# Performance work log

Hardware: AMD Instinct MI355X
Metric: run time of the kernel (lower is better)

The kernel has to match this reference:

```python
import jax, jax.numpy as jnp
import numpy as np

PAD = 1      # init_kwargs: padding
STRIDE = 1   # init_kwargs: stride


def setup_inputs() -> dict:
    key = jax.random.key(0)
    k1, k2 = jax.random.split(key)
    # x: [C=4, H=4096, W=4096] input feature map (no batch dim in original module)
    x = jax.random.normal(k1, (4, 4096, 4096), dtype=jnp.float32)
    # kernel: [cout=4, cin=4, h=3, w=3] learned conv weight (nn.Parameter)
    kernel = jax.random.normal(k2, (4, 4, 3, 3), dtype=jnp.float32)
    return {"x": x, "kernel": kernel}


def reference(x, kernel):
    # Faithful math: zero-pad by PAD on all four spatial sides, then a direct
    # cross-correlation (torch conv semantics) with stride STRIDE.
    # Original loops over output pixels; here it's a single fused conv primitive.
    out = jax.lax.conv_general_dilated(
        x[None],                      # [1, C, H, W]
        kernel,                       # [cout, cin, h, w]
        window_strides=(STRIDE, STRIDE),
        padding=[(PAD, PAD), (PAD, PAD)],
        dimension_numbers=("NCHW", "OIHW", "NCHW"),
    )
    return out[0]                     # [cout, hout, wout]
```

## Files before the change

kernel.cpp:

```cpp
#include <hip/hip_runtime.h>


#define IW 4096
#define IH 4096
constexpr long long HWsz = (long long)IH * IW;

typedef float v4f __attribute__((ext_vector_type(4)));

#define LROW 1028

__device__ __forceinline__ void gload_lds16(const float* g, float* l) {
    __builtin_amdgcn_global_load_lds(
        (const __attribute__((address_space(1))) char*)g,
        (__attribute__((address_space(3))) char*)l, 16, 0, 0);
}
__device__ __forceinline__ void gload_lds4(const float* g, float* l) {
    __builtin_amdgcn_global_load_lds(
        (const __attribute__((address_space(1))) char*)g,
        (__attribute__((address_space(3))) char*)l, 4, 0, 0);
}

__device__ __forceinline__ void stage(const float* __restrict__ xin, int ci,
                                      float (*rbuf)[LROW], float* hbuf,
                                      int y0, int X0, int w, int l) {
    const float* plane = xin + (long long)ci * HWsz;
    const int xg = X0 + 256 * w + 4 * l;
    #pragma unroll
    for (int r = 0; r < 6; ++r) {
        int yy = y0 - 1 + r;
        int yc = yy < 0 ? 0 : (yy >= IH ? IH - 1 : yy);
        gload_lds16(plane + (long long)yc * IW + xg, &rbuf[r][256 * w]);
    }
    if (l < 3) {
        const int s   = 3 * w + l;
        const int r   = s >> 1;
        const int sid = s & 1;
        int yy = y0 - 1 + r;
        int yc = yy < 0 ? 0 : (yy >= IH ? IH - 1 : yy);
        int x  = sid ? (X0 + 1024) : (X0 - 1);
        int xc = x < 0 ? 0 : (x >= IW ? IW - 1 : x);
        gload_lds4(plane + (long long)yc * IW + xc, &hbuf[3 * w]);
    }
}

__device__ __forceinline__ void compute_ci(float acc[4][4][4],
                                           const float (*rbuf)[LROW],
                                           const float* hbuf,
                                           const float* __restrict__ wt, int ci,
                                           int y0, int t, bool xlo, bool xhi) {
    #pragma unroll
    for (int dy = 0; dy < 6; ++dy) {
        const int yy = y0 - 1 + dy;
        if (yy >= 0 && yy < IH) {
            const v4f a = *reinterpret_cast<const v4f*>(&rbuf[dy][4 * t]);
            float L = (t == 0)   ? hbuf[2 * dy]     : rbuf[dy][4 * t - 1];
            float R = (t == 255) ? hbuf[2 * dy + 1] : rbuf[dy][4 * t + 4];
            if (t == 0 && xlo)   L = 0.f;
            if (t == 255 && xhi) R = 0.f;
            float vv[6] = {L, a.x, a.y, a.z, a.w, R};
            #pragma unroll
            for (int rk = 0; rk < 3; ++rk) {
                const int o = dy - rk;
                if (o >= 0 && o < 4) {
                    #pragma unroll
                    for (int co = 0; co < 4; ++co) {
                        #pragma unroll
                        for (int kx = 0; kx < 3; ++kx) {
                            const float w = wt[((co * 4 + ci) * 3 + rk) * 3 + kx];
                            #pragma unroll
                            for (int p = 0; p < 4; ++p)
                                acc[o][co][p] = fmaf(w, vv[p + kx], acc[o][co][p]);
                        }
                    }
                }
            }
        }
    }
}

__global__ __launch_bounds__(256) void conv3x3_kernel(
    const float* __restrict__ xin,
    const float* __restrict__ wt,
    float* __restrict__ out)
{
    __shared__ __align__(16) float rows[2][6][LROW];
    __shared__ float halo[2][12];

    const int bid = blockIdx.x;
    const int swz = (bid & 7) * 512 + (bid >> 3);
    const int rowblk = swz >> 2;
    const int xq     = swz & 3;
    const int y0     = rowblk << 2;
    const int X0     = xq << 10;
    const int t      = (int)threadIdx.x;
    const int w      = t >> 6, l = t & 63;
    const bool xlo   = (X0 == 0);
    const bool xhi   = (X0 + 1024 == IW);

    float acc[4][4][4];
    #pragma unroll
    for (int o = 0; o < 4; ++o)
        #pragma unroll
        for (int co = 0; co < 4; ++co)
            #pragma unroll
            for (int p = 0; p < 4; ++p) acc[o][co][p] = 0.f;

    stage(xin, 0, rows[0], halo[0], y0, X0, w, l);

    #pragma unroll 1
    for (int ci = 0; ci < 4; ++ci) {
        const int cur = ci & 1;
        if (ci < 3) {
            stage(xin, ci + 1, rows[cur ^ 1], halo[cur ^ 1], y0, X0, w, l);
            asm volatile("s_waitcnt vmcnt(7)\n\ts_barrier" ::: "memory");
        } else {
            asm volatile("s_waitcnt vmcnt(0)\n\ts_barrier" ::: "memory");
        }
        compute_ci(acc, rows[cur], halo[cur], wt, ci, y0, t, xlo, xhi);
        if (ci < 3)
            asm volatile("s_barrier" ::: "memory");
    }

    const int x0g = X0 + 4 * t;
    #pragma unroll
    for (int o = 0; o < 4; ++o) {
        const long long obase = (long long)(y0 + o) * IW + x0g;
        #pragma unroll
        for (int co = 0; co < 4; ++co) {
            v4f ov;
            ov.x = acc[o][co][0]; ov.y = acc[o][co][1];
            ov.z = acc[o][co][2]; ov.w = acc[o][co][3];
            __builtin_nontemporal_store(ov,
                reinterpret_cast<v4f*>(out + co * HWsz + obase));
        }
    }
}

extern "C" void kernel_launch(void* const* d_in, const int* in_sizes, int n_in,
                              void* d_out, int out_size, void* d_ws, size_t ws_size,
                              hipStream_t stream) {
    const float* xin = (const float*)d_in[0];
    const float* wt  = (const float*)d_in[1];
    float* out       = (float*)d_out;

    dim3 grid(4096), block(256);
    hipLaunchKernelGGL(conv3x3_kernel, grid, block, 0, stream, xin, wt, out);
}
```

Baseline: 97.87 us.

## Give each wavefront private LDS staging buffers and drop block barriers

The shared 1024-wide LDS row buffer is split into four 256-wide per-wavefront buffers, and each wave now loads its own halo columns. Because no wave reads another wave's data, the s_barrier calls are replaced by per-wave waitcnts, so waves no longer stall on each other between input channels. In exchange each wave loads extra halo elements, and correctness now depends on waitcnt ordering within a wave instead of block barriers.

```diff
diff --git a/kernel.cpp b/kernel.cpp
--- a/kernel.cpp
+++ b/kernel.cpp
@@ -6,8 +6,6 @@
 constexpr long long HWsz = (long long)IH * IW;
 
 typedef float v4f __attribute__((ext_vector_type(4)));
-
-#define LROW 1028
 
 __device__ __forceinline__ void gload_lds16(const float* g, float* l) {
     __builtin_amdgcn_global_load_lds(
@@ -21,42 +19,40 @@
 }
 
 __device__ __forceinline__ void stage(const float* __restrict__ xin, int ci,
-                                      float (*rbuf)[LROW], float* hbuf,
-                                      int y0, int X0, int w, int l) {
+                                      float (*rbuf)[256], float* hbuf,
+                                      int y0, int xw, int l) {
     const float* plane = xin + (long long)ci * HWsz;
-    const int xg = X0 + 256 * w + 4 * l;
     #pragma unroll
     for (int r = 0; r < 6; ++r) {
         int yy = y0 - 1 + r;
         int yc = yy < 0 ? 0 : (yy >= IH ? IH - 1 : yy);
-        gload_lds16(plane + (long long)yc * IW + xg, &rbuf[r][256 * w]);
+        gload_lds16(plane + (long long)yc * IW + (xw + 4 * l), &rbuf[r][0]);
     }
-    if (l < 3) {
-        const int s   = 3 * w + l;
-        const int r   = s >> 1;
-        const int sid = s & 1;
+    if (l < 12) {
+        const int r   = l >> 1;
+        const int sid = l & 1;
         int yy = y0 - 1 + r;
         int yc = yy < 0 ? 0 : (yy >= IH ? IH - 1 : yy);
-        int x  = sid ? (X0 + 1024) : (X0 - 1);
+        int x  = sid ? (xw + 256) : (xw - 1);
         int xc = x < 0 ? 0 : (x >= IW ? IW - 1 : x);
-        gload_lds4(plane + (long long)yc * IW + xc, &hbuf[3 * w]);
+        gload_lds4(plane + (long long)yc * IW + xc, &hbuf[0]);
     }
 }
 
 __device__ __forceinline__ void compute_ci(float acc[4][4][4],
-                                           const float (*rbuf)[LROW],
+                                           const float (*rbuf)[256],
                                            const float* hbuf,
                                            const float* __restrict__ wt, int ci,
-                                           int y0, int t, bool xlo, bool xhi) {
+                                           int y0, int l, bool xlo, bool xhi) {
     #pragma unroll
     for (int dy = 0; dy < 6; ++dy) {
         const int yy = y0 - 1 + dy;
         if (yy >= 0 && yy < IH) {
-            const v4f a = *reinterpret_cast<const v4f*>(&rbuf[dy][4 * t]);
-            float L = (t == 0)   ? hbuf[2 * dy]     : rbuf[dy][4 * t - 1];
-            float R = (t == 255) ? hbuf[2 * dy + 1] : rbuf[dy][4 * t + 4];
-            if (t == 0 && xlo)   L = 0.f;
-            if (t == 255 && xhi) R = 0.f;
+            const v4f a = *reinterpret_cast<const v4f*>(&rbuf[dy][4 * l]);
+            const float L = (l == 0)  ? (xlo ? 0.f : hbuf[2 * dy])
+                                      : rbuf[dy][4 * l - 1];
+            const float R = (l == 63) ? (xhi ? 0.f : hbuf[2 * dy + 1])
+                                      : rbuf[dy][4 * l + 4];
             float vv[6] = {L, a.x, a.y, a.z, a.w, R};
             #pragma unroll
             for (int rk = 0; rk < 3; ++rk) {
@@ -83,8 +79,8 @@
     const float* __restrict__ wt,
     float* __restrict__ out)
 {
-    __shared__ __align__(16) float rows[2][6][LROW];
-    __shared__ float halo[2][12];
+    __shared__ __align__(16) float rows[4][2][6][256];
+    __shared__ float halo[4][2][12];
 
     const int bid = blockIdx.x;
     const int swz = (bid & 7) * 512 + (bid >> 3);
@@ -94,8 +90,9 @@
     const int X0     = xq << 10;
     const int t      = (int)threadIdx.x;
     const int w      = t >> 6, l = t & 63;
-    const bool xlo   = (X0 == 0);
-    const bool xhi   = (X0 + 1024 == IW);
+    const int xw     = X0 + 256 * w;
+    const bool xlo   = (xw == 0);
+    const bool xhi   = (xw + 256 == IW);
 
     float acc[4][4][4];
     #pragma unroll
@@ -105,20 +102,19 @@
             #pragma unroll
             for (int p = 0; p < 4; ++p) acc[o][co][p] = 0.f;
 
-    stage(xin, 0, rows[0], halo[0], y0, X0, w, l);
+    stage(xin, 0, rows[w][0], halo[w][0], y0, xw, l);
 
     #pragma unroll 1
     for (int ci = 0; ci < 4; ++ci) {
         const int cur = ci & 1;
         if (ci < 3) {
-            stage(xin, ci + 1, rows[cur ^ 1], halo[cur ^ 1], y0, X0, w, l);
-            asm volatile("s_waitcnt vmcnt(7)\n\ts_barrier" ::: "memory");
+            asm volatile("s_waitcnt lgkmcnt(0)" ::: "memory");
+            stage(xin, ci + 1, rows[w][cur ^ 1], halo[w][cur ^ 1], y0, xw, l);
+            asm volatile("s_waitcnt vmcnt(7)" ::: "memory");
         } else {
-            asm volatile("s_waitcnt vmcnt(0)\n\ts_barrier" ::: "memory");
+            asm volatile("s_waitcnt vmcnt(0)" ::: "memory");
         }
-        compute_ci(acc, rows[cur], halo[cur], wt, ci, y0, t, xlo, xhi);
-        if (ci < 3)
-            asm volatile("s_barrier" ::: "memory");
+        compute_ci(acc, rows[w][cur], halo[w][cur], wt, ci, y0, l, xlo, xhi);
     }
 
     const int x0g = X0 + 4 * t;
```

New measurement: 104.9 us. +7.2%, slower.

## Retile conv to 8x512 blocks and fetch halo columns directly from global

Applied to the files above, without the earlier changes.

Each block now covers 8 output rows by 512 columns instead of 4 rows by 1024 columns. Each half of the block computes 4 rows from a shared 10-row LDS staging buffer. Before, every 4 output rows needed 6 input rows; now every 8 output rows need 10, which lowers redundant input reads. The separate LDS halo staging is dropped; each wave loads the left and right halo pixels straight from global memory inside the compute loop, using wave-uniform addresses. This simplifies staging, but it adds global loads on the compute path that may stall it.

```diff
diff --git a/kernel.cpp b/kernel.cpp
--- a/kernel.cpp
+++ b/kernel.cpp
@@ -7,56 +7,47 @@
 
 typedef float v4f __attribute__((ext_vector_type(4)));
 
-#define LROW 1028
-
 __device__ __forceinline__ void gload_lds16(const float* g, float* l) {
     __builtin_amdgcn_global_load_lds(
         (const __attribute__((address_space(1))) char*)g,
         (__attribute__((address_space(3))) char*)l, 16, 0, 0);
 }
-__device__ __forceinline__ void gload_lds4(const float* g, float* l) {
-    __builtin_amdgcn_global_load_lds(
-        (const __attribute__((address_space(1))) char*)g,
-        (__attribute__((address_space(3))) char*)l, 4, 0, 0);
-}
 
 __device__ __forceinline__ void stage(const float* __restrict__ xin, int ci,
-                                      float (*rbuf)[LROW], float* hbuf,
-                                      int y0, int X0, int w, int l) {
+                                      float (*rbuf)[512], int y0, int X0,
+                                      int w, int l) {
     const float* plane = xin + (long long)ci * HWsz;
-    const int xg = X0 + 256 * w + 4 * l;
     #pragma unroll
-    for (int r = 0; r < 6; ++r) {
+    for (int k = 0; k < 5; ++k) {
+        const int c = 5 * w + k;
+        const int r = c >> 1;
+        const int h = c & 1;
         int yy = y0 - 1 + r;
         int yc = yy < 0 ? 0 : (yy >= IH ? IH - 1 : yy);
-        gload_lds16(plane + (long long)yc * IW + xg, &rbuf[r][256 * w]);
-    }
-    if (l < 3) {
-        const int s   = 3 * w + l;
-        const int r   = s >> 1;
-        const int sid = s & 1;
-        int yy = y0 - 1 + r;
-        int yc = yy < 0 ? 0 : (yy >= IH ? IH - 1 : yy);
-        int x  = sid ? (X0 + 1024) : (X0 - 1);
-        int xc = x < 0 ? 0 : (x >= IW ? IW - 1 : x);
-        gload_lds4(plane + (long long)yc * IW + xc, &hbuf[3 * w]);
+        gload_lds16(plane + (long long)yc * IW + (X0 + 256 * h + 4 * l),
+                    &rbuf[r][256 * h]);
     }
 }
 
 __device__ __forceinline__ void compute_ci(float acc[4][4][4],
-                                           const float (*rbuf)[LROW],
-                                           const float* hbuf,
-                                           const float* __restrict__ wt, int ci,
-                                           int y0, int t, bool xlo, bool xhi) {
+                                           const float (*rbuf)[512],
+                                           const float* __restrict__ xin,
+                                           const float* __restrict__ wt,
+                                           int ci, int y0, int X0,
+                                           int p_u, int tx) {
+    const float* plane = xin + (long long)ci * HWsz;
     #pragma unroll
     for (int dy = 0; dy < 6; ++dy) {
-        const int yy = y0 - 1 + dy;
+        const int r  = 4 * p_u + dy;
+        const int yy = y0 - 1 + r;
         if (yy >= 0 && yy < IH) {
-            const v4f a = *reinterpret_cast<const v4f*>(&rbuf[dy][4 * t]);
-            float L = (t == 0)   ? hbuf[2 * dy]     : rbuf[dy][4 * t - 1];
-            float R = (t == 255) ? hbuf[2 * dy + 1] : rbuf[dy][4 * t + 4];
-            if (t == 0 && xlo)   L = 0.f;
-            if (t == 255 && xhi) R = 0.f;
+            const float hL = (X0 > 0)
+                ? plane[(long long)yy * IW + X0 - 1]   : 0.f;
+            const float hR = (X0 + 512 < IW)
+                ? plane[(long long)yy * IW + X0 + 512] : 0.f;
+            const v4f a = *reinterpret_cast<const v4f*>(&rbuf[r][4 * tx]);
+            const float L = (tx == 0)   ? hL : rbuf[r][4 * tx - 1];
+            const float R = (tx == 127) ? hR : rbuf[r][4 * tx + 4];
             float vv[6] = {L, a.x, a.y, a.z, a.w, R};
             #pragma unroll
             for (int rk = 0; rk < 3; ++rk) {
@@ -83,19 +74,18 @@
     const float* __restrict__ wt,
     float* __restrict__ out)
 {
-    __shared__ __align__(16) float rows[2][6][LROW];
-    __shared__ float halo[2][12];
+    __shared__ __align__(16) float rows[2][10][512];
 
     const int bid = blockIdx.x;
     const int swz = (bid & 7) * 512 + (bid >> 3);
-    const int rowblk = swz >> 2;
-    const int xq     = swz & 3;
-    const int y0     = rowblk << 2;
-    const int X0     = xq << 10;
+    const int rowblk = swz >> 3;
+    const int xs     = swz & 7;
+    const int y0     = rowblk << 3;
+    const int X0     = xs << 9;
     const int t      = (int)threadIdx.x;
     const int w      = t >> 6, l = t & 63;
-    const bool xlo   = (X0 == 0);
-    const bool xhi   = (X0 + 1024 == IW);
+    const int tx     = t & 127;
+    const int p_u    = __builtin_amdgcn_readfirstlane(t >> 7);
 
     float acc[4][4][4];
     #pragma unroll
@@ -105,26 +95,26 @@
             #pragma unroll
             for (int p = 0; p < 4; ++p) acc[o][co][p] = 0.f;
 
-    stage(xin, 0, rows[0], halo[0], y0, X0, w, l);
+    stage(xin, 0, rows[0], y0, X0, w, l);
 
     #pragma unroll 1
     for (int ci = 0; ci < 4; ++ci) {
         const int cur = ci & 1;
         if (ci < 3) {
-            stage(xin, ci + 1, rows[cur ^ 1], halo[cur ^ 1], y0, X0, w, l);
-            asm volatile("s_waitcnt vmcnt(7)\n\ts_barrier" ::: "memory");
+            stage(xin, ci + 1, rows[cur ^ 1], y0, X0, w, l);
+            asm volatile("s_waitcnt vmcnt(5)\n\ts_barrier" ::: "memory");
         } else {
             asm volatile("s_waitcnt vmcnt(0)\n\ts_barrier" ::: "memory");
         }
-        compute_ci(acc, rows[cur], halo[cur], wt, ci, y0, t, xlo, xhi);
+        compute_ci(acc, rows[cur], xin, wt, ci, y0, X0, p_u, tx);
         if (ci < 3)
             asm volatile("s_barrier" ::: "memory");
     }
 
-    const int x0g = X0 + 4 * t;
+    const int x0g = X0 + 4 * tx;
     #pragma unroll
     for (int o = 0; o < 4; ++o) {
-        const long long obase = (long long)(y0 + o) * IW + x0g;
+        const long long obase = (long long)(y0 + 4 * p_u + o) * IW + x0g;
         #pragma unroll
         for (int co = 0; co < 4; ++co) {
             v4f ov;
```

After: 95.79 us. 1.02x faster.
